# Kernel tuning notes

Hardware: AMD Instinct MI355X
Metric: run time of the kernel (lower is better)

## Reference

```python
import jax, jax.numpy as jnp
import numpy as np

B, S, D, H, F, E = 8, 1024, 1024, 16, 3584, 2
HD = D // H
NUM_LABELS = 2
EPS = 1e-6


def setup_inputs() -> dict:
    key = jax.random.key(0)
    ks = jax.random.split(key, 10)
    w = lambda k, shape: jax.random.normal(k, shape, jnp.float32) * 0.02
    return {
        "hidden_states": jax.random.normal(ks[0], (B, S, D), jnp.float32),
        "ln1_w": jnp.ones((D,), jnp.float32),
        "q_w": w(ks[1], (D, D)),
        "k_w": w(ks[2], (D, D)),
        "v_w": w(ks[3], (D, D)),
        "o_w": w(ks[4], (D, D)),
        "ln2_w": jnp.ones((D,), jnp.float32),
        "router_w": w(ks[5], (D, E)),
        "gate_w": w(ks[6], (E, D, F)),
        "up_w": w(ks[7], (E, D, F)),
        "down_w": w(ks[8], (E, F, D)),
        "final_ln_w": jnp.ones((D,), jnp.float32),
        "score_w": w(ks[9], (D, NUM_LABELS)),
    }


def rmsnorm(x, w):
    var = jnp.mean(jnp.square(x), axis=-1, keepdims=True)
    return x * jax.lax.rsqrt(var + EPS) * w


def reference(hidden_states, ln1_w, q_w, k_w, v_w, o_w, ln2_w, router_w,
              gate_w, up_w, down_w, final_ln_w, score_w):
    x = hidden_states  # [B,S,D]
    # --- attention block (Jamba attention: no RoPE, no bias, causal) ---
    res = x
    h = rmsnorm(x, ln1_w)
    q = (h @ q_w).reshape(B, S, H, HD).transpose(0, 2, 1, 3)  # [B,H,S,HD]
    k = (h @ k_w).reshape(B, S, H, HD).transpose(0, 2, 1, 3)
    v = (h @ v_w).reshape(B, S, H, HD).transpose(0, 2, 1, 3)
    scores = jnp.einsum("bhqd,bhkd->bhqk", q, k) / np.sqrt(HD).astype(np.float32)
    causal = jnp.tril(jnp.ones((S, S), bool))
    scores = jnp.where(causal, scores, jnp.finfo(jnp.float32).min)
    attn = jax.nn.softmax(scores, axis=-1)
    ctx = jnp.einsum("bhqk,bhkd->bhqd", attn, v)
    attn_out = ctx.transpose(0, 2, 1, 3).reshape(B, S, D) @ o_w
    x = res + attn_out
    # --- top-1 MoE FFN (Jamba: softmax router, top-k, NO renormalization) ---
    res = x
    h = rmsnorm(x, ln2_w).reshape(B * S, D)
    router_logits = h @ router_w  # [N,E]
    probs = jax.nn.softmax(router_logits.astype(jnp.float32), axis=-1)
    top_w = jnp.max(probs, axis=-1)       # top-1 weight
    sel = jnp.argmax(probs, axis=-1)      # selected expert id
    moe = jnp.zeros_like(h)
    for e in range(E):  # fixed tiny loop over experts
        y = (jax.nn.silu(h @ gate_w[e]) * (h @ up_w[e])) @ down_w[e]
        moe = moe + jnp.where(sel == e, top_w, 0.0)[:, None] * y
    x = res + moe.reshape(B, S, D)
    # --- final RMSNorm + score head on first token ---
    x = rmsnorm(x, final_ln_w)
    logits = x[:, 0, :] @ score_w  # [B, NUM_LABELS]
    return logits
```

## Files before the change

### kernel.cpp

```cpp
#include <hip/hip_runtime.h>
#include <math.h>

#define B 8
#define S 1024
#define D 1024
#define F 3584

#define KSV 64
#define CHV 16
#define KSG 32
#define CHG 32
#define KSD 112
#define CHD 32

#define FMA4(A, s, W) { (A).x += (s)*(W).x; (A).y += (s)*(W).y; (A).z += (s)*(W).z; (A).w += (s)*(W).w; }

__device__ __forceinline__ float block_sum256(float v, volatile float* buf) {
  #pragma unroll
  for (int o = 32; o; o >>= 1) v += __shfl_down(v, o);
  __syncthreads();
  if ((threadIdx.x & 63) == 0) buf[threadIdx.x >> 6] = v;
  __syncthreads();
  return buf[0] + buf[1] + buf[2] + buf[3];
}

__global__ void k_rms1(const float* __restrict__ hs, const float* __restrict__ w,
                       float* __restrict__ h1) {
  __shared__ float buf[4];
  int b = blockIdx.x;
  int idx = threadIdx.x * 4;
  float4 x = *(const float4*)(hs + (size_t)b * S * D + idx);
  float ss = x.x * x.x + x.y * x.y + x.z * x.z + x.w * x.w;
  float tot = block_sum256(ss, buf);
  float sc = rsqrtf(tot * (1.f / (float)D) + 1e-6f);
  float4 wv = *(const float4*)(w + idx);
  float4 o;
  o.x = x.x * sc * wv.x; o.y = x.y * sc * wv.y;
  o.z = x.z * sc * wv.z; o.w = x.w * sc * wv.w;
  *(float4*)(h1 + b * D + idx) = o;
}

__global__ __launch_bounds__(64) void k_mvp(const float* __restrict__ X,
                                            const float* __restrict__ W,
                                            float* __restrict__ P) {
  __shared__ float xs[8 * CHV];
  int i0 = blockIdx.y * CHV;
  for (int t = threadIdx.x; t < 8 * CHV; t += 64)
    xs[t] = X[(t >> 4) * D + i0 + (t & 15)];
  __syncthreads();
  int j = (blockIdx.x * 64 + threadIdx.x) * 4;
  const float4* Wp = (const float4*)(W + (size_t)i0 * D + j);
  const int st = D / 4;
  float4 acc[8];
  #pragma unroll
  for (int bb = 0; bb < 8; bb++) acc[bb] = make_float4(0.f, 0.f, 0.f, 0.f);
  #pragma unroll 1
  for (int ii = 0; ii < CHV; ii += 8) {
    float4 w0 = Wp[0 * st], w1 = Wp[1 * st], w2 = Wp[2 * st], w3 = Wp[3 * st];
    float4 w4 = Wp[4 * st], w5 = Wp[5 * st], w6 = Wp[6 * st], w7 = Wp[7 * st];
    Wp += 8 * st;
    #pragma unroll
    for (int bb = 0; bb < 8; bb++) {
      float4 xa = *(const float4*)(xs + bb * CHV + ii);
      float4 xb = *(const float4*)(xs + bb * CHV + ii + 4);
      FMA4(acc[bb], xa.x, w0); FMA4(acc[bb], xa.y, w1);
      FMA4(acc[bb], xa.z, w2); FMA4(acc[bb], xa.w, w3);
      FMA4(acc[bb], xb.x, w4); FMA4(acc[bb], xb.y, w5);
      FMA4(acc[bb], xb.z, w6); FMA4(acc[bb], xb.w, w7);
    }
  }
  #pragma unroll
  for (int bb = 0; bb < 8; bb++)
    *(float4*)(P + ((size_t)blockIdx.y * 8 + bb) * D + j) = acc[bb];
}

__global__ void k_red8k(const float* __restrict__ P, float* __restrict__ v0) {
  int o = blockIdx.x * 256 + threadIdx.x;
  const float4* P4 = (const float4*)P;
  float4 s = make_float4(0.f, 0.f, 0.f, 0.f);
  #pragma unroll 8
  for (int p = 0; p < KSV; p++) {
    float4 v = P4[(size_t)p * (8 * D / 4) + o];
    s.x += v.x; s.y += v.y; s.z += v.z; s.w += v.w;
  }
  ((float4*)v0)[o] = s;
}

__global__ void k_mid(const float* __restrict__ hs, const float* __restrict__ Op,
                      const float* __restrict__ ln2, const float* __restrict__ rw,
                      float* __restrict__ xr, float* __restrict__ h2,
                      float* __restrict__ topw, int* __restrict__ sel) {
  __shared__ float buf[4];
  int b = blockIdx.x;
  int idx = threadIdx.x * 4;
  float4 x = *(const float4*)(hs + (size_t)b * S * D + idx);
  #pragma unroll 8
  for (int p = 0; p < KSV; p++) {
    float4 v = *(const float4*)(Op + ((size_t)p * 8 + b) * D + idx);
    x.x += v.x; x.y += v.y; x.z += v.z; x.w += v.w;
  }
  *(float4*)(xr + b * D + idx) = x;
  float ss = x.x * x.x + x.y * x.y + x.z * x.z + x.w * x.w;
  float tot = block_sum256(ss, buf);
  float sc = rsqrtf(tot * (1.f / (float)D) + 1e-6f);
  float4 wv = *(const float4*)(ln2 + idx);
  float4 h;
  h.x = x.x * sc * wv.x; h.y = x.y * sc * wv.y;
  h.z = x.z * sc * wv.z; h.w = x.w * sc * wv.w;
  *(float4*)(h2 + b * D + idx) = h;
  float r0 = h.x * rw[idx * 2] + h.y * rw[(idx + 1) * 2] +
             h.z * rw[(idx + 2) * 2] + h.w * rw[(idx + 3) * 2];
  float r1 = h.x * rw[idx * 2 + 1] + h.y * rw[(idx + 1) * 2 + 1] +
             h.z * rw[(idx + 2) * 2 + 1] + h.w * rw[(idx + 3) * 2 + 1];
  r0 = block_sum256(r0, buf);
  r1 = block_sum256(r1, buf);
  if (threadIdx.x == 0) {
    float m = fmaxf(r0, r1);
    float e0 = __expf(r0 - m), e1 = __expf(r1 - m);
    float inv = 1.f / (e0 + e1);
    float p0 = e0 * inv, p1 = e1 * inv;
    topw[b] = fmaxf(p0, p1);
    sel[b] = (p1 > p0) ? 1 : 0;
  }
}

__global__ __launch_bounds__(64) void k_gateup(const float* __restrict__ h2,
                                               const float* __restrict__ gw,
                                               const float* __restrict__ uw,
                                               float* __restrict__ Gp,
                                               float* __restrict__ Up) {
  __shared__ float xs[8 * CHG];
  int e = blockIdx.z >> 1, m = blockIdx.z & 1;
  int i0 = blockIdx.y * CHG;
  for (int t = threadIdx.x; t < 8 * CHG; t += 64)
    xs[t] = h2[(t >> 5) * D + i0 + (t & 31)];
  __syncthreads();
  const float* wsrc = m ? uw : gw;
  float* out = m ? Up : Gp;
  int j = (blockIdx.x * 64 + threadIdx.x) * 4;
  const float4* Wp = (const float4*)(wsrc + (size_t)e * D * F + (size_t)i0 * F + j);
  const int st = F / 4;
  float4 acc[8];
  #pragma unroll
  for (int bb = 0; bb < 8; bb++) acc[bb] = make_float4(0.f, 0.f, 0.f, 0.f);
  #pragma unroll 1
  for (int ii = 0; ii < CHG; ii += 8) {
    float4 w0 = Wp[0 * st], w1 = Wp[1 * st], w2 = Wp[2 * st], w3 = Wp[3 * st];
    float4 w4 = Wp[4 * st], w5 = Wp[5 * st], w6 = Wp[6 * st], w7 = Wp[7 * st];
    Wp += 8 * st;
    #pragma unroll
    for (int bb = 0; bb < 8; bb++) {
      float4 xa = *(const float4*)(xs + bb * CHG + ii);
      float4 xb = *(const float4*)(xs + bb * CHG + ii + 4);
      FMA4(acc[bb], xa.x, w0); FMA4(acc[bb], xa.y, w1);
      FMA4(acc[bb], xa.z, w2); FMA4(acc[bb], xa.w, w3);
      FMA4(acc[bb], xb.x, w4); FMA4(acc[bb], xb.y, w5);
      FMA4(acc[bb], xb.z, w6); FMA4(acc[bb], xb.w, w7);
    }
  }
  #pragma unroll
  for (int bb = 0; bb < 8; bb++)
    *(float4*)(out + (((size_t)blockIdx.y * 2 + e) * 8 + bb) * F + j) = acc[bb];
}

__global__ void k_silu_red(const float* __restrict__ Gp, const float* __restrict__ Up,
                           float* __restrict__ g) {
  int o = blockIdx.x * 256 + threadIdx.x;
  const float4* G4 = (const float4*)Gp;
  const float4* U4 = (const float4*)Up;
  float4 ga = make_float4(0.f, 0.f, 0.f, 0.f);
  float4 ua = make_float4(0.f, 0.f, 0.f, 0.f);
  #pragma unroll 8
  for (int p = 0; p < KSG; p++) {
    float4 gv = G4[(size_t)p * (2 * 8 * F / 4) + o];
    float4 uv = U4[(size_t)p * (2 * 8 * F / 4) + o];
    ga.x += gv.x; ga.y += gv.y; ga.z += gv.z; ga.w += gv.w;
    ua.x += uv.x; ua.y += uv.y; ua.z += uv.z; ua.w += uv.w;
  }
  float4 r;
  r.x = (ga.x / (1.f + __expf(-ga.x))) * ua.x;
  r.y = (ga.y / (1.f + __expf(-ga.y))) * ua.y;
  r.z = (ga.z / (1.f + __expf(-ga.z))) * ua.z;
  r.w = (ga.w / (1.f + __expf(-ga.w))) * ua.w;
  ((float4*)g)[o] = r;
}

__global__ __launch_bounds__(64) void k_down(const float* __restrict__ g,
                                             const float* __restrict__ dw,
                                             float* __restrict__ Dp) {
  __shared__ float xs[8 * CHD];
  int e = blockIdx.z;
  int i0 = blockIdx.y * CHD;
  const float* X = g + (size_t)e * 8 * F;
  for (int t = threadIdx.x; t < 8 * CHD; t += 64)
    xs[t] = X[(t >> 5) * F + i0 + (t & 31)];
  __syncthreads();
  int j = (blockIdx.x * 64 + threadIdx.x) * 4;
  const float4* Wp = (const float4*)(dw + (size_t)e * F * D + (size_t)i0 * D + j);
  const int st = D / 4;
  float4 acc[8];
  #pragma unroll
  for (int bb = 0; bb < 8; bb++) acc[bb] = make_float4(0.f, 0.f, 0.f, 0.f);
  #pragma unroll 1
  for (int ii = 0; ii < CHD; ii += 8) {
    float4 w0 = Wp[0 * st], w1 = Wp[1 * st], w2 = Wp[2 * st], w3 = Wp[3 * st];
    float4 w4 = Wp[4 * st], w5 = Wp[5 * st], w6 = Wp[6 * st], w7 = Wp[7 * st];
    Wp += 8 * st;
    #pragma unroll
    for (int bb = 0; bb < 8; bb++) {
      float4 xa = *(const float4*)(xs + bb * CHD + ii);
      float4 xb = *(const float4*)(xs + bb * CHD + ii + 4);
      FMA4(acc[bb], xa.x, w0); FMA4(acc[bb], xa.y, w1);
      FMA4(acc[bb], xa.z, w2); FMA4(acc[bb], xa.w, w3);
      FMA4(acc[bb], xb.x, w4); FMA4(acc[bb], xb.y, w5);
      FMA4(acc[bb], xb.z, w6); FMA4(acc[bb], xb.w, w7);
    }
  }
  #pragma unroll
  for (int bb = 0; bb < 8; bb++)
    *(float4*)(Dp + (((size_t)blockIdx.y * 2 + e) * 8 + bb) * D + j) = acc[bb];
}

__global__ void k_final(const float* __restrict__ xr, const float* __restrict__ Dp,
                        const float* __restrict__ topw, const int* __restrict__ sel,
                        const float* __restrict__ flw, const float* __restrict__ sw,
                        float* __restrict__ out) {
  __shared__ float buf[4];
  int b = blockIdx.x;
  int e = sel[b];
  float tw = topw[b];
  int idx = threadIdx.x * 4;
  float4 y = make_float4(0.f, 0.f, 0.f, 0.f);
  #pragma unroll 8
  for (int p = 0; p < KSD; p++) {
    float4 v = *(const float4*)(Dp + (((size_t)p * 2 + e) * 8 + b) * D + idx);
    y.x += v.x; y.y += v.y; y.z += v.z; y.w += v.w;
  }
  float4 x = *(const float4*)(xr + b * D + idx);
  x.x += tw * y.x; x.y += tw * y.y; x.z += tw * y.z; x.w += tw * y.w;
  float ss = x.x * x.x + x.y * x.y + x.z * x.z + x.w * x.w;
  float tot = block_sum256(ss, buf);
  float sc = rsqrtf(tot * (1.f / (float)D) + 1e-6f);
  float4 wv = *(const float4*)(flw + idx);
  float n0 = x.x * sc * wv.x, n1 = x.y * sc * wv.y;
  float n2 = x.z * sc * wv.z, n3 = x.w * sc * wv.w;
  float l0 = n0 * sw[idx * 2] + n1 * sw[(idx + 1) * 2] +
             n2 * sw[(idx + 2) * 2] + n3 * sw[(idx + 3) * 2];
  float l1 = n0 * sw[idx * 2 + 1] + n1 * sw[(idx + 1) * 2 + 1] +
             n2 * sw[(idx + 2) * 2 + 1] + n3 * sw[(idx + 3) * 2 + 1];
  l0 = block_sum256(l0, buf);
  l1 = block_sum256(l1, buf);
  if (threadIdx.x == 0) { out[b * 2 + 0] = l0; out[b * 2 + 1] = l1; }
}

extern "C" void kernel_launch(void* const* d_in, const int* in_sizes, int n_in,
                              void* d_out, int out_size, void* d_ws, size_t ws_size,
                              hipStream_t stream) {
  const float* hs  = (const float*)d_in[0];
  const float* ln1 = (const float*)d_in[1];
  const float* vw  = (const float*)d_in[4];
  const float* ow  = (const float*)d_in[5];
  const float* ln2 = (const float*)d_in[6];
  const float* rw  = (const float*)d_in[7];
  const float* gw  = (const float*)d_in[8];
  const float* uw  = (const float*)d_in[9];
  const float* dw  = (const float*)d_in[10];
  const float* flw = (const float*)d_in[11];
  const float* sw  = (const float*)d_in[12];

  float* ws = (float*)d_ws;
  float* h1   = ws;
  float* Vp   = ws + 8192;
  float* v0   = ws + 532480;
  float* Op   = ws + 540672;
  float* xr   = ws + 1064960;
  float* h2   = ws + 1073152;
  float* Gp   = ws + 1081344;
  float* Up   = ws + 2916352;
  float* g    = ws + 4751360;
  float* Dp   = ws + 4808704;
  float* topw = ws + 6643712;
  int*   sel  = (int*)(ws + 6643720);

  k_rms1<<<8, 256, 0, stream>>>(hs, ln1, h1);
  k_mvp<<<dim3(4, KSV), 64, 0, stream>>>(h1, vw, Vp);
  k_red8k<<<8, 256, 0, stream>>>(Vp, v0);
  k_mvp<<<dim3(4, KSV), 64, 0, stream>>>(v0, ow, Op);
  k_mid<<<8, 256, 0, stream>>>(hs, Op, ln2, rw, xr, h2, topw, sel);
  k_gateup<<<dim3(F / 256, KSG, 4), 64, 0, stream>>>(h2, gw, uw, Gp, Up);
  k_silu_red<<<56, 256, 0, stream>>>(Gp, Up, g);
  k_down<<<dim3(4, KSD, 2), 64, 0, stream>>>(g, dw, Dp);
  k_final<<<8, 256, 0, stream>>>(xr, Dp, topw, sel, flw, sw, (float*)d_out);
}
```

Baseline: 209.2 us.

## Use 256-thread blocks with register double-buffered weight loads in matvec kernels

The three split-K matvec kernels (V/O projection, gate/up, down) now run 256-thread blocks instead of 64-thread blocks. Each thread also prefetches the next 8 weight rows into registers before doing FMAs on the current ones, so more loads are in flight. The gate and up partials are merged into one buffer indexed by (chunk, matrix, expert), and the SiLU reduction reads it with the new indexing. The aim is better latency hiding on the memory-bound weight streaming, at the cost of more registers per thread and fewer, larger blocks.

```diff
diff --git a/kernel.cpp b/kernel.cpp
--- a/kernel.cpp
+++ b/kernel.cpp
@@ -9,11 +9,23 @@
 #define KSV 64
 #define CHV 16
 #define KSG 32
-#define CHG 32
 #define KSD 112
-#define CHD 32
-
+#define CH32 32
+
+#define LD4(p) (*(const float4*)(p))
 #define FMA4(A, s, W) { (A).x += (s)*(W).x; (A).y += (s)*(W).y; (A).z += (s)*(W).z; (A).w += (s)*(W).w; }
+
+#define BB8(bb, ACC, XS, CH, koff) { \
+  float4 xa = LD4((XS) + (bb)*(CH) + (koff)); \
+  float4 xb = LD4((XS) + (bb)*(CH) + (koff) + 4); \
+  FMA4(ACC, xa.x, w0); FMA4(ACC, xa.y, w1); FMA4(ACC, xa.z, w2); FMA4(ACC, xa.w, w3); \
+  FMA4(ACC, xb.x, w4); FMA4(ACC, xb.y, w5); FMA4(ACC, xb.z, w6); FMA4(ACC, xb.w, w7); }
+
+#define ALL8(XS, CH, koff) \
+  BB8(0, acc0, XS, CH, koff) BB8(1, acc1, XS, CH, koff) \
+  BB8(2, acc2, XS, CH, koff) BB8(3, acc3, XS, CH, koff) \
+  BB8(4, acc4, XS, CH, koff) BB8(5, acc5, XS, CH, koff) \
+  BB8(6, acc6, XS, CH, koff) BB8(7, acc7, XS, CH, koff)
 
 __device__ __forceinline__ float block_sum256(float v, volatile float* buf) {
   #pragma unroll
@@ -29,55 +41,49 @@
   __shared__ float buf[4];
   int b = blockIdx.x;
   int idx = threadIdx.x * 4;
-  float4 x = *(const float4*)(hs + (size_t)b * S * D + idx);
+  float4 x = LD4(hs + (size_t)b * S * D + idx);
   float ss = x.x * x.x + x.y * x.y + x.z * x.z + x.w * x.w;
   float tot = block_sum256(ss, buf);
   float sc = rsqrtf(tot * (1.f / (float)D) + 1e-6f);
-  float4 wv = *(const float4*)(w + idx);
+  float4 wv = LD4(w + idx);
   float4 o;
   o.x = x.x * sc * wv.x; o.y = x.y * sc * wv.y;
   o.z = x.z * sc * wv.z; o.w = x.w * sc * wv.w;
   *(float4*)(h1 + b * D + idx) = o;
 }
 
-__global__ __launch_bounds__(64) void k_mvp(const float* __restrict__ X,
-                                            const float* __restrict__ W,
-                                            float* __restrict__ P) {
+__global__ __launch_bounds__(256, 2) void k_mvp(const float* __restrict__ X,
+                                                const float* __restrict__ W,
+                                                float* __restrict__ P) {
   __shared__ float xs[8 * CHV];
-  int i0 = blockIdx.y * CHV;
-  for (int t = threadIdx.x; t < 8 * CHV; t += 64)
-    xs[t] = X[(t >> 4) * D + i0 + (t & 15)];
-  __syncthreads();
-  int j = (blockIdx.x * 64 + threadIdx.x) * 4;
+  int i0 = blockIdx.x * CHV;
+  if (threadIdx.x < 8 * CHV)
+    xs[threadIdx.x] = X[(threadIdx.x >> 4) * D + i0 + (threadIdx.x & 15)];
+  __syncthreads();
+  int j = threadIdx.x * 4;
   const float4* Wp = (const float4*)(W + (size_t)i0 * D + j);
   const int st = D / 4;
-  float4 acc[8];
-  #pragma unroll
-  for (int bb = 0; bb < 8; bb++) acc[bb] = make_float4(0.f, 0.f, 0.f, 0.f);
-  #pragma unroll 1
-  for (int ii = 0; ii < CHV; ii += 8) {
-    float4 w0 = Wp[0 * st], w1 = Wp[1 * st], w2 = Wp[2 * st], w3 = Wp[3 * st];
-    float4 w4 = Wp[4 * st], w5 = Wp[5 * st], w6 = Wp[6 * st], w7 = Wp[7 * st];
-    Wp += 8 * st;
-    #pragma unroll
-    for (int bb = 0; bb < 8; bb++) {
-      float4 xa = *(const float4*)(xs + bb * CHV + ii);
-      float4 xb = *(const float4*)(xs + bb * CHV + ii + 4);
-      FMA4(acc[bb], xa.x, w0); FMA4(acc[bb], xa.y, w1);
-      FMA4(acc[bb], xa.z, w2); FMA4(acc[bb], xa.w, w3);
-      FMA4(acc[bb], xb.x, w4); FMA4(acc[bb], xb.y, w5);
-      FMA4(acc[bb], xb.z, w6); FMA4(acc[bb], xb.w, w7);
-    }
-  }
-  #pragma unroll
-  for (int bb = 0; bb < 8; bb++)
-    *(float4*)(P + ((size_t)blockIdx.y * 8 + bb) * D + j) = acc[bb];
+  float4 acc0 = {0,0,0,0}, acc1 = {0,0,0,0}, acc2 = {0,0,0,0}, acc3 = {0,0,0,0};
+  float4 acc4 = {0,0,0,0}, acc5 = {0,0,0,0}, acc6 = {0,0,0,0}, acc7 = {0,0,0,0};
+  {
+    float4 w0 = Wp[0*st], w1 = Wp[1*st], w2 = Wp[2*st], w3 = Wp[3*st];
+    float4 w4 = Wp[4*st], w5 = Wp[5*st], w6 = Wp[6*st], w7 = Wp[7*st];
+    float4 v0 = Wp[8*st], v1 = Wp[9*st], v2 = Wp[10*st], v3 = Wp[11*st];
+    float4 v4 = Wp[12*st], v5 = Wp[13*st], v6 = Wp[14*st], v7 = Wp[15*st];
+    ALL8(xs, CHV, 0);
+    w0 = v0; w1 = v1; w2 = v2; w3 = v3; w4 = v4; w5 = v5; w6 = v6; w7 = v7;
+    ALL8(xs, CHV, 8);
+  }
+  #define MV_ST(bb, ACC) *(float4*)(P + ((size_t)blockIdx.x * 8 + (bb)) * D + j) = ACC;
+  MV_ST(0, acc0) MV_ST(1, acc1) MV_ST(2, acc2) MV_ST(3, acc3)
+  MV_ST(4, acc4) MV_ST(5, acc5) MV_ST(6, acc6) MV_ST(7, acc7)
+  #undef MV_ST
 }
 
 __global__ void k_red8k(const float* __restrict__ P, float* __restrict__ v0) {
   int o = blockIdx.x * 256 + threadIdx.x;
   const float4* P4 = (const float4*)P;
-  float4 s = make_float4(0.f, 0.f, 0.f, 0.f);
+  float4 s = {0,0,0,0};
   #pragma unroll 8
   for (int p = 0; p < KSV; p++) {
     float4 v = P4[(size_t)p * (8 * D / 4) + o];
@@ -93,17 +99,17 @@
   __shared__ float buf[4];
   int b = blockIdx.x;
   int idx = threadIdx.x * 4;
-  float4 x = *(const float4*)(hs + (size_t)b * S * D + idx);
+  float4 x = LD4(hs + (size_t)b * S * D + idx);
   #pragma unroll 8
   for (int p = 0; p < KSV; p++) {
-    float4 v = *(const float4*)(Op + ((size_t)p * 8 + b) * D + idx);
+    float4 v = LD4(Op + ((size_t)p * 8 + b) * D + idx);
     x.x += v.x; x.y += v.y; x.z += v.z; x.w += v.w;
   }
   *(float4*)(xr + b * D + idx) = x;
   float ss = x.x * x.x + x.y * x.y + x.z * x.z + x.w * x.w;
   float tot = block_sum256(ss, buf);
   float sc = rsqrtf(tot * (1.f / (float)D) + 1e-6f);
-  float4 wv = *(const float4*)(ln2 + idx);
+  float4 wv = LD4(ln2 + idx);
   float4 h;
   h.x = x.x * sc * wv.x; h.y = x.y * sc * wv.y;
   h.z = x.z * sc * wv.z; h.w = x.w * sc * wv.w;
@@ -124,56 +130,51 @@
   }
 }
 
-__global__ __launch_bounds__(64) void k_gateup(const float* __restrict__ h2,
-                                               const float* __restrict__ gw,
-                                               const float* __restrict__ uw,
-                                               float* __restrict__ Gp,
-                                               float* __restrict__ Up) {
-  __shared__ float xs[8 * CHG];
-  int e = blockIdx.z >> 1, m = blockIdx.z & 1;
-  int i0 = blockIdx.y * CHG;
-  for (int t = threadIdx.x; t < 8 * CHG; t += 64)
-    xs[t] = h2[(t >> 5) * D + i0 + (t & 31)];
-  __syncthreads();
-  const float* wsrc = m ? uw : gw;
-  float* out = m ? Up : Gp;
-  int j = (blockIdx.x * 64 + threadIdx.x) * 4;
-  const float4* Wp = (const float4*)(wsrc + (size_t)e * D * F + (size_t)i0 * F + j);
+__global__ __launch_bounds__(256, 2) void k_gateup(const float* __restrict__ h2,
+                                                   const float* __restrict__ gw,
+                                                   const float* __restrict__ uw,
+                                                   float* __restrict__ Pgu) {
+  __shared__ float xs[8 * CH32];
+  int i0 = blockIdx.y * CH32;
+  xs[threadIdx.x] = h2[(threadIdx.x >> 5) * D + i0 + (threadIdx.x & 31)];
+  __syncthreads();
+  int c = blockIdx.x * 1024 + threadIdx.x * 4;
+  int m = c / F;
+  int j = c - m * F;
+  const float* base = (m < 2 ? gw : uw) + (size_t)(m & 1) * D * F;
+  const float4* Wp = (const float4*)(base + (size_t)i0 * F + j);
   const int st = F / 4;
-  float4 acc[8];
+  float4 acc0 = {0,0,0,0}, acc1 = {0,0,0,0}, acc2 = {0,0,0,0}, acc3 = {0,0,0,0};
+  float4 acc4 = {0,0,0,0}, acc5 = {0,0,0,0}, acc6 = {0,0,0,0}, acc7 = {0,0,0,0};
+  float4 w0 = Wp[0*st], w1 = Wp[1*st], w2 = Wp[2*st], w3 = Wp[3*st];
+  float4 w4 = Wp[4*st], w5 = Wp[5*st], w6 = Wp[6*st], w7 = Wp[7*st];
+  Wp += 8 * st;
   #pragma unroll
-  for (int bb = 0; bb < 8; bb++) acc[bb] = make_float4(0.f, 0.f, 0.f, 0.f);
-  #pragma unroll 1
-  for (int ii = 0; ii < CHG; ii += 8) {
-    float4 w0 = Wp[0 * st], w1 = Wp[1 * st], w2 = Wp[2 * st], w3 = Wp[3 * st];
-    float4 w4 = Wp[4 * st], w5 = Wp[5 * st], w6 = Wp[6 * st], w7 = Wp[7 * st];
+  for (int t = 0; t < CH32 / 8 - 1; t++) {
+    float4 n0 = Wp[0*st], n1 = Wp[1*st], n2 = Wp[2*st], n3 = Wp[3*st];
+    float4 n4 = Wp[4*st], n5 = Wp[5*st], n6 = Wp[6*st], n7 = Wp[7*st];
     Wp += 8 * st;
-    #pragma unroll
-    for (int bb = 0; bb < 8; bb++) {
-      float4 xa = *(const float4*)(xs + bb * CHG + ii);
-      float4 xb = *(const float4*)(xs + bb * CHG + ii + 4);
-      FMA4(acc[bb], xa.x, w0); FMA4(acc[bb], xa.y, w1);
-      FMA4(acc[bb], xa.z, w2); FMA4(acc[bb], xa.w, w3);
-      FMA4(acc[bb], xb.x, w4); FMA4(acc[bb], xb.y, w5);
-      FMA4(acc[bb], xb.z, w6); FMA4(acc[bb], xb.w, w7);
-    }
-  }
-  #pragma unroll
-  for (int bb = 0; bb < 8; bb++)
-    *(float4*)(out + (((size_t)blockIdx.y * 2 + e) * 8 + bb) * F + j) = acc[bb];
-}
-
-__global__ void k_silu_red(const float* __restrict__ Gp, const float* __restrict__ Up,
-                           float* __restrict__ g) {
+    ALL8(xs, CH32, t * 8);
+    w0 = n0; w1 = n1; w2 = n2; w3 = n3; w4 = n4; w5 = n5; w6 = n6; w7 = n7;
+  }
+  ALL8(xs, CH32, CH32 - 8);
+  #define GU_ST(bb, ACC) \
+    *(float4*)(Pgu + (((size_t)blockIdx.y * 4 + m) * 8 + (bb)) * F + j) = ACC;
+  GU_ST(0, acc0) GU_ST(1, acc1) GU_ST(2, acc2) GU_ST(3, acc3)
+  GU_ST(4, acc4) GU_ST(5, acc5) GU_ST(6, acc6) GU_ST(7, acc7)
+  #undef GU_ST
+}
+
+__global__ void k_silu_red(const float* __restrict__ Pgu, float* __restrict__ g) {
   int o = blockIdx.x * 256 + threadIdx.x;
-  const float4* G4 = (const float4*)Gp;
-  const float4* U4 = (const float4*)Up;
-  float4 ga = make_float4(0.f, 0.f, 0.f, 0.f);
-  float4 ua = make_float4(0.f, 0.f, 0.f, 0.f);
-  #pragma unroll 8
-  for (int p = 0; p < KSG; p++) {
-    float4 gv = G4[(size_t)p * (2 * 8 * F / 4) + o];
-    float4 uv = U4[(size_t)p * (2 * 8 * F / 4) + o];
+  int e = o / (8 * F / 4);
+  int rem = o - e * (8 * F / 4);
+  const float4* P4 = (const float4*)Pgu;
+  float4 ga = {0,0,0,0}, ua = {0,0,0,0};
+  #pragma unroll 8
+  for (int kc = 0; kc < KSG; kc++) {
+    float4 gv = P4[(size_t)(kc * 4 + e)     * (8 * F / 4) + rem];
+    float4 uv = P4[(size_t)(kc * 4 + 2 + e) * (8 * F / 4) + rem];
     ga.x += gv.x; ga.y += gv.y; ga.z += gv.z; ga.w += gv.w;
     ua.x += uv.x; ua.y += uv.y; ua.z += uv.z; ua.w += uv.w;
   }
@@ -185,40 +186,36 @@
   ((float4*)g)[o] = r;
 }
 
-__global__ __launch_bounds__(64) void k_down(const float* __restrict__ g,
-                                             const float* __restrict__ dw,
-                                             float* __restrict__ Dp) {
-  __shared__ float xs[8 * CHD];
-  int e = blockIdx.z;
-  int i0 = blockIdx.y * CHD;
-  const float* X = g + (size_t)e * 8 * F;
-  for (int t = threadIdx.x; t < 8 * CHD; t += 64)
-    xs[t] = X[(t >> 5) * F + i0 + (t & 31)];
-  __syncthreads();
-  int j = (blockIdx.x * 64 + threadIdx.x) * 4;
+__global__ __launch_bounds__(256, 2) void k_down(const float* __restrict__ g,
+                                                 const float* __restrict__ dw,
+                                                 float* __restrict__ Dp) {
+  __shared__ float xs[8 * CH32];
+  int e = blockIdx.x;
+  int i0 = blockIdx.y * CH32;
+  xs[threadIdx.x] = g[(size_t)e * 8 * F + (threadIdx.x >> 5) * F + i0 + (threadIdx.x & 31)];
+  __syncthreads();
+  int j = threadIdx.x * 4;
   const float4* Wp = (const float4*)(dw + (size_t)e * F * D + (size_t)i0 * D + j);
   const int st = D / 4;
-  float4 acc[8];
+  float4 acc0 = {0,0,0,0}, acc1 = {0,0,0,0}, acc2 = {0,0,0,0}, acc3 = {0,0,0,0};
+  float4 acc4 = {0,0,0,0}, acc5 = {0,0,0,0}, acc6 = {0,0,0,0}, acc7 = {0,0,0,0};
+  float4 w0 = Wp[0*st], w1 = Wp[1*st], w2 = Wp[2*st], w3 = Wp[3*st];
+  float4 w4 = Wp[4*st], w5 = Wp[5*st], w6 = Wp[6*st], w7 = Wp[7*st];
+  Wp += 8 * st;
   #pragma unroll
-  for (int bb = 0; bb < 8; bb++) acc[bb] = make_float4(0.f, 0.f, 0.f, 0.f);
-  #pragma unroll 1
-  for (int ii = 0; ii < CHD; ii += 8) {
-    float4 w0 = Wp[0 * st], w1 = Wp[1 * st], w2 = Wp[2 * st], w3 = Wp[3 * st];
-    float4 w4 = Wp[4 * st], w5 = Wp[5 * st], w6 = Wp[6 * st], w7 = Wp[7 * st];
+  for (int t = 0; t < CH32 / 8 - 1; t++) {
+    float4 n0 = Wp[0*st], n1 = Wp[1*st], n2 = Wp[2*st], n3 = Wp[3*st];
+    float4 n4 = Wp[4*st], n5 = Wp[5*st], n6 = Wp[6*st], n7 = Wp[7*st];
     Wp += 8 * st;
-    #pragma unroll
-    for (int bb = 0; bb < 8; bb++) {
-      float4 xa = *(const float4*)(xs + bb * CHD + ii);
-      float4 xb = *(const float4*)(xs + bb * CHD + ii + 4);
-      FMA4(acc[bb], xa.x, w0); FMA4(acc[bb], xa.y, w1);
-      FMA4(acc[bb], xa.z, w2); FMA4(acc[bb], xa.w, w3);
-      FMA4(acc[bb], xb.x, w4); FMA4(acc[bb], xb.y, w5);
-      FMA4(acc[bb], xb.z, w6); FMA4(acc[bb], xb.w, w7);
-    }
-  }
-  #pragma unroll
-  for (int bb = 0; bb < 8; bb++)
-    *(float4*)(Dp + (((size_t)blockIdx.y * 2 + e) * 8 + bb) * D + j) = acc[bb];
+    ALL8(xs, CH32, t * 8);
+    w0 = n0; w1 = n1; w2 = n2; w3 = n3; w4 = n4; w5 = n5; w6 = n6; w7 = n7;
+  }
+  ALL8(xs, CH32, CH32 - 8);
+  #define DN_ST(bb, ACC) \
+    *(float4*)(Dp + (((size_t)blockIdx.y * 2 + e) * 8 + (bb)) * D + j) = ACC;
+  DN_ST(0, acc0) DN_ST(1, acc1) DN_ST(2, acc2) DN_ST(3, acc3)
+  DN_ST(4, acc4) DN_ST(5, acc5) DN_ST(6, acc6) DN_ST(7, acc7)
+  #undef DN_ST
 }
 
 __global__ void k_final(const float* __restrict__ xr, const float* __restrict__ Dp,
@@ -230,18 +227,18 @@
   int e = sel[b];
   float tw = topw[b];
   int idx = threadIdx.x * 4;
-  float4 y = make_float4(0.f, 0.f, 0.f, 0.f);
+  float4 y = {0,0,0,0};
   #pragma unroll 8
   for (int p = 0; p < KSD; p++) {
-    float4 v = *(const float4*)(Dp + (((size_t)p * 2 + e) * 8 + b) * D + idx);
+    float4 v = LD4(Dp + (((size_t)p * 2 + e) * 8 + b) * D + idx);
     y.x += v.x; y.y += v.y; y.z += v.z; y.w += v.w;
   }
-  float4 x = *(const float4*)(xr + b * D + idx);
+  float4 x = LD4(xr + b * D + idx);
   x.x += tw * y.x; x.y += tw * y.y; x.z += tw * y.z; x.w += tw * y.w;
   float ss = x.x * x.x + x.y * x.y + x.z * x.z + x.w * x.w;
   float tot = block_sum256(ss, buf);
   float sc = rsqrtf(tot * (1.f / (float)D) + 1e-6f);
-  float4 wv = *(const float4*)(flw + idx);
+  float4 wv = LD4(flw + idx);
   float n0 = x.x * sc * wv.x, n1 = x.y * sc * wv.y;
   float n2 = x.z * sc * wv.z, n3 = x.w * sc * wv.w;
   float l0 = n0 * sw[idx * 2] + n1 * sw[(idx + 1) * 2] +
@@ -275,20 +272,19 @@
   float* Op   = ws + 540672;
   float* xr   = ws + 1064960;
   float* h2   = ws + 1073152;
-  float* Gp   = ws + 1081344;
-  float* Up   = ws + 2916352;
+  float* Pgu  = ws + 1081344;
   float* g    = ws + 4751360;
   float* Dp   = ws + 4808704;
   float* topw = ws + 6643712;
   int*   sel  = (int*)(ws + 6643720);
 
   k_rms1<<<8, 256, 0, stream>>>(hs, ln1, h1);
-  k_mvp<<<dim3(4, KSV), 64, 0, stream>>>(h1, vw, Vp);
+  k_mvp<<<KSV, 256, 0, stream>>>(h1, vw, Vp);
   k_red8k<<<8, 256, 0, stream>>>(Vp, v0);
-  k_mvp<<<dim3(4, KSV), 64, 0, stream>>>(v0, ow, Op);
+  k_mvp<<<KSV, 256, 0, stream>>>(v0, ow, Op);
   k_mid<<<8, 256, 0, stream>>>(hs, Op, ln2, rw, xr, h2, topw, sel);
-  k_gateup<<<dim3(F / 256, KSG, 4), 64, 0, stream>>>(h2, gw, uw, Gp, Up);
-  k_silu_red<<<56, 256, 0, stream>>>(Gp, Up, g);
-  k_down<<<dim3(4, KSD, 2), 64, 0, stream>>>(g, dw, Dp);
+  k_gateup<<<dim3(14, KSG), 256, 0, stream>>>(h2, gw, uw, Pgu);
+  k_silu_red<<<56, 256, 0, stream>>>(Pgu, g);
+  k_down<<<dim3(2, KSD), 256, 0, stream>>>(g, dw, Dp);
   k_final<<<8, 256, 0, stream>>>(xr, Dp, topw, sel, flw, sw, (float*)d_out);
 }
```

Measured after the change: 205.7 us. About the same (-1.7%).
